# Optimization experiments

Measured on AMD Instinct MI355X. Metric: run time of the kernel, lower is better.

The kernel has to match this reference:

```python
import jax, jax.numpy as jnp
import numpy as np

B, T, E, H = 8, 2048, 1024, 64  # batch, seq_len(=block_size), embedding_size, head_size


def setup_inputs() -> dict:
    key = jax.random.key(0)
    k1, k2, k3, k4, k5 = jax.random.split(key, 5)
    x = jax.random.normal(k1, (B, T, E), dtype=jnp.float32)
    Wk = jax.random.normal(k2, (H, E), dtype=jnp.float32) * 0.02
    Wq = jax.random.normal(k3, (H, E), dtype=jnp.float32) * 0.02
    Wv = jax.random.normal(k4, (H, E), dtype=jnp.float32) * 0.02
    attention_mask = jax.random.randint(k5, (B, T), 0, 2).astype(jnp.int32)
    return {"x": x, "Wk": Wk, "Wq": Wq, "Wv": Wv, "attention_mask": attention_mask}


def reference(x, Wk, Wq, Wv, attention_mask):
    # Linear projections (nn.Linear with no bias: y = x @ W.T)
    k = jnp.einsum('bte,he->bth', x, Wk)
    q = jnp.einsum('bte,he->bth', x, Wq)
    v = jnp.einsum('bte,he->bth', x, Wv)
    scale = v.shape[2] ** -0.5  # head_size^-0.5, faithful to v.shape[2]**(-0.5)
    wei = jnp.einsum('bqh,bkh->bqk', q, k) * scale  # [B,T,T]
    # Causal mask (tril buffer) AND padding outer-product mask; the double-precision
    # outer product in the original just tests nonzero-ness, so a boolean AND is exact.
    causal = jnp.tril(jnp.ones((T, T), dtype=bool))  # [T,T]
    pad = (attention_mask[:, :, None] * attention_mask[:, None, :]) != 0  # [B,T,T]
    wei = jnp.where(causal[None, :, :] & pad, wei, -jnp.inf)
    wei = jax.nn.softmax(wei, axis=-1)
    wei = jnp.nan_to_num(wei)  # fully-masked rows -> 0 (matches torch.nan_to_num)
    # dropout in eval mode -> identity
    out = jnp.einsum('bqk,bkh->bqh', wei, v)
    return out
```

## Files before the change

kernel.cpp:

```cpp
#include <hip/hip_runtime.h>
#include <hip/hip_bf16.h>

typedef __bf16 bf16x8 __attribute__((ext_vector_type(8)));
typedef __bf16 bf16x4 __attribute__((ext_vector_type(4)));
typedef float  f32x4  __attribute__((ext_vector_type(4)));

#define LDP  72
#define KLDP 72
#define VLDP 72
#define PLDP 72

#define BAR() { asm volatile("s_waitcnt lgkmcnt(0)" ::: "memory"); __builtin_amdgcn_s_barrier(); }

__global__ __launch_bounds__(256) void wconv_kernel(
    const float* __restrict__ Wk, const float* __restrict__ Wq,
    const float* __restrict__ Wv, const int* __restrict__ mask,
    __bf16* __restrict__ wbf, unsigned* __restrict__ maskw)
{
    if (blockIdx.x == 192) {
        for (int wdx = threadIdx.x; wdx < 512; wdx += 256) {
            unsigned wv = 0;
            #pragma unroll
            for (int bit = 0; bit < 32; bit++)
                wv |= (mask[wdx * 32 + bit] != 0 ? 1u : 0u) << bit;
            maskw[wdx] = wv;
        }
        return;
    }
    int idx = blockIdx.x * 256 + threadIdx.x;
    int row = idx >> 8;
    int c4  = idx & 255;
    const float* wp = (row < 64) ? Wk + (size_t)row * 1024
                    : (row < 128) ? Wq + (size_t)(row - 64) * 1024
                                  : Wv + (size_t)(row - 128) * 1024;
    float4 f = *reinterpret_cast<const float4*>(wp + c4 * 4);
    bf16x4 v; v[0] = (__bf16)f.x; v[1] = (__bf16)f.y; v[2] = (__bf16)f.z; v[3] = (__bf16)f.w;
    *reinterpret_cast<bf16x4*>(&wbf[(size_t)row * 1024 + c4 * 4]) = v;
}

__global__ __launch_bounds__(1024) void proj_kernel(
    const float* __restrict__ x, const __bf16* __restrict__ wbf,
    __bf16* __restrict__ kbuf, __bf16* __restrict__ qbuf, __bf16* __restrict__ vtbuf)
{
    __shared__ __align__(16) __bf16 Slds[2][256 * LDP];
    __shared__ __align__(16) __bf16 Vtl[64 * LDP];

    const int tid  = threadIdx.x;
    const int lane = tid & 63;
    const int wid  = tid >> 6;
    const int wm   = wid >> 2;
    const int wn   = wid & 3;
    const int mbase = blockIdx.x * 64;

    const int cl = lane & 15;
    const int e0 = (lane >> 4) * 8;
    const int r0 = (lane >> 4) * 4;

    const int arow = tid >> 4, acg = tid & 15;
    const float* aptr = x + (size_t)(mbase + arow) * 1024 + acg * 4;

    float4 a0, a1;
    bf16x4 w0[3], w1[3];

#define ISSUE(aset, wset, kb) { \
    aset = *reinterpret_cast<const float4*>(aptr + (kb)); \
    _Pragma("unroll") \
    for (int i_ = 0; i_ < 3; i_++) { \
        int c_ = i_ * 1024 + tid; \
        wset[i_] = *reinterpret_cast<const bf16x4*>(&wbf[(size_t)(c_ >> 4) * 1024 + (kb) + (c_ & 15) * 4]); \
    } }

#define COMMIT(aset, wset, bufi) { \
    bf16x4 av_; \
    av_[0] = (__bf16)aset.x; av_[1] = (__bf16)aset.y; av_[2] = (__bf16)aset.z; av_[3] = (__bf16)aset.w; \
    *reinterpret_cast<bf16x4*>(&Slds[bufi][arow * LDP + acg * 4]) = av_; \
    _Pragma("unroll") \
    for (int i_ = 0; i_ < 3; i_++) { \
        int c_ = i_ * 1024 + tid; \
        *reinterpret_cast<bf16x4*>(&Slds[bufi][(64 + (c_ >> 4)) * LDP + (c_ & 15) * 4]) = wset[i_]; \
    } }

    f32x4 acc[3];
    #pragma unroll
    for (int n = 0; n < 3; n++) acc[n] = (f32x4){0.f, 0.f, 0.f, 0.f};

    ISSUE(a0, w0, 0);
    COMMIT(a0, w0, 0);
    ISSUE(a1, w1, 64);
    BAR();

    #pragma unroll 2
    for (int j = 0; j < 16; j++) {
        if (j < 14) {
            if (j & 1) { ISSUE(a1, w1, (j + 2) * 64); }
            else       { ISSUE(a0, w0, (j + 2) * 64); }
        }
        const __bf16* buf = Slds[j & 1];
        #pragma unroll
        for (int kk = 0; kk < 2; kk++) {
            bf16x8 a = *reinterpret_cast<const bf16x8*>(&buf[(wm * 16 + cl) * LDP + kk * 32 + e0]);
            #pragma unroll
            for (int nf = 0; nf < 3; nf++) {
                bf16x8 b = *reinterpret_cast<const bf16x8*>(&buf[(64 + wn * 48 + nf * 16 + cl) * LDP + kk * 32 + e0]);
                acc[nf] = __builtin_amdgcn_mfma_f32_16x16x32_bf16(a, b, acc[nf], 0, 0, 0);
            }
        }
        if (j < 15) {
            if (j & 1) { COMMIT(a0, w0, 0); }
            else       { COMMIT(a1, w1, 1); }
            BAR();
        }
    }
#undef ISSUE
#undef COMMIT

    #pragma unroll
    for (int nf = 0; nf < 3; nf++) {
        int c = wn * 48 + nf * 16 + cl;
        #pragma unroll
        for (int r = 0; r < 4; r++) {
            int mrel = wm * 16 + r0 + r;
            float v = acc[nf][r];
            if (c < 64)        kbuf[(size_t)(mbase + mrel) * 64 + c]         = (__bf16)v;
            else if (c < 128)  qbuf[(size_t)(mbase + mrel) * 64 + (c - 64)]  = (__bf16)v;
            else               Vtl[(c - 128) * LDP + mrel]                   = (__bf16)v;
        }
    }
    __syncthreads();
    {
        int b   = mbase >> 11;
        int tof = mbase & 2047;
        int h   = tid >> 4;
        int seg = tid & 15;
        bf16x4 v4 = *reinterpret_cast<const bf16x4*>(&Vtl[h * LDP + seg * 4]);
        *reinterpret_cast<bf16x4*>(&vtbuf[(size_t)b * 64 * 2048 + (size_t)h * 2048 + tof + seg * 4]) = v4;
    }
}

__global__ __launch_bounds__(128) void attn_kernel(
    const __bf16* __restrict__ qbuf, const __bf16* __restrict__ kbuf,
    const __bf16* __restrict__ vtbuf, const unsigned* __restrict__ maskw,
    float* __restrict__ out, float* __restrict__ accpart, float* __restrict__ mlpart,
    int nsplit, int tps)
{
    __shared__ __align__(16) __bf16 Klds[64 * KLDP];
    __shared__ __align__(16) __bf16 Vlds[64 * VLDP];
    __shared__ __align__(16) __bf16 Plds[2][2][16 * PLDP];

    const int tid  = threadIdx.x;
    const int lane = tid & 63;
    const int w    = tid >> 6;
    const int wg   = blockIdx.x;
    const int b    = wg & 7;
    const int rr_  = wg >> 3;
    const int qt   = rr_ & 31;
    const int sp   = rr_ >> 5;

    const int jbeg = sp * tps;
    const int jend = min((sp + 1) * tps, qt + 1);

    if (nsplit > 1 && jbeg >= jend) {
        for (int i = tid; i < 64; i += 128) {
            size_t mo = ((size_t)(b * nsplit + sp) * 2048 + qt * 64 + i) * 2;
            mlpart[mo] = -INFINITY; mlpart[mo + 1] = 0.f;
        }
        return;
    }

    const int cl = lane & 15;
    const int e0 = (lane >> 4) * 8;
    const int r0 = (lane >> 4) * 4;
    const int qs0 = qt * 64 + w * 16 + cl;
    const int qs1 = qs0 + 32;

    bf16x8 aq0[2], aq1[2];
    #pragma unroll
    for (int kk = 0; kk < 2; kk++) {
        aq0[kk] = *reinterpret_cast<const bf16x8*>(&qbuf[((size_t)b * 2048 + qs0) * 64 + kk * 32 + e0]);
        aq1[kk] = *reinterpret_cast<const bf16x8*>(&qbuf[((size_t)b * 2048 + qs1) * 64 + kk * 32 + e0]);
    }

    float m0 = -INFINITY, l0 = 0.f, m1 = -INFINITY, l1 = 0.f;
    f32x4 acc0[4], acc1[4];
    #pragma unroll
    for (int hf = 0; hf < 4; hf++) { acc0[hf] = (f32x4){0.f,0.f,0.f,0.f}; acc1[hf] = (f32x4){0.f,0.f,0.f,0.f}; }

    const __bf16* kb  = kbuf  + (size_t)b * 2048 * 64;
    const __bf16* vtb = vtbuf + (size_t)b * 64 * 2048;

    const int srow = tid >> 1;
    const int sc   = (tid & 1) * 32;
    bf16x8 stk[4], stv[4];

#define KV_ISSUE(jj) { _Pragma("unroll") for (int i_ = 0; i_ < 4; i_++) { \
    stk[i_] = *reinterpret_cast<const bf16x8*>(&kb[(size_t)((jj) * 64 + srow) * 64 + sc + i_ * 8]); \
    stv[i_] = *reinterpret_cast<const bf16x8*>(&vtb[(size_t)srow * 2048 + (jj) * 64 + sc + i_ * 8]); } }

#define KV_COMMIT() { _Pragma("unroll") for (int i_ = 0; i_ < 4; i_++) { \
    *reinterpret_cast<bf16x8*>(&Klds[srow * KLDP + sc + i_ * 8]) = stk[i_]; \
    *reinterpret_cast<bf16x8*>(&Vlds[srow * VLDP + sc + i_ * 8]) = stv[i_]; } }

#define SOFTMAX(S, mS, lS, accS, qsS, su) { \
    float tmax = -INFINITY; \
    _Pragma("unroll") for (int jf = 0; jf < 4; jf++) { \
        unsigned mw = (jf < 2) ? mw0 : mw1; \
        _Pragma("unroll") for (int r = 0; r < 4; r++) { \
            int kvl = jf * 16 + r0 + r; \
            bool ok = ((mw >> (kvl & 31)) & 1u) && (j * 64 + kvl <= qsS); \
            float sv = S[jf][r] * 0.125f; \
            sv = ok ? sv : -INFINITY; \
            S[jf][r] = sv; tmax = fmaxf(tmax, sv); } } \
    tmax = fmaxf(tmax, __shfl_xor(tmax, 16)); \
    tmax = fmaxf(tmax, __shfl_xor(tmax, 32)); \
    float mn = fmaxf(mS, tmax); \
    float alpha = (mn == -INFINITY) ? 1.0f : __expf(mS - mn); \
    float rs = 0.f; \
    _Pragma("unroll") for (int jf = 0; jf < 4; jf++) \
        _Pragma("unroll") for (int r = 0; r < 4; r++) { \
            float p = (mn == -INFINITY) ? 0.f : __expf(S[jf][r] - mn); \
            S[jf][r] = p; rs += p; } \
    rs += __shfl_xor(rs, 16); \
    rs += __shfl_xor(rs, 32); \
    lS = lS * alpha + rs; mS = mn; \
    _Pragma("unroll") for (int hf = 0; hf < 4; hf++) \
        _Pragma("unroll") for (int r = 0; r < 4; r++) accS[hf][r] *= alpha; \
    _Pragma("unroll") for (int jf = 0; jf < 4; jf++) { \
        bf16x4 p4; \
        _Pragma("unroll") for (int r = 0; r < 4; r++) p4[r] = (__bf16)S[jf][r]; \
        *reinterpret_cast<bf16x4*>(&Plds[w][su][cl * PLDP + jf * 16 + r0]) = p4; } }

    const int nt = jend - jbeg;
    KV_ISSUE(jbeg);
    KV_COMMIT();
    if (nt > 1) KV_ISSUE(jbeg + 1);
    BAR();

    for (int t = 0; t < nt; t++) {
        const int j = jbeg + t;

        f32x4 s0[4], s1[4];
        #pragma unroll
        for (int jf = 0; jf < 4; jf++) {
            f32x4 t0 = (f32x4){0.f,0.f,0.f,0.f}, t1 = (f32x4){0.f,0.f,0.f,0.f};
            #pragma unroll
            for (int kk = 0; kk < 2; kk++) {
                bf16x8 bk = *reinterpret_cast<const bf16x8*>(&Klds[(jf * 16 + cl) * KLDP + kk * 32 + e0]);
                t0 = __builtin_amdgcn_mfma_f32_16x16x32_bf16(bk, aq0[kk], t0, 0, 0, 0);
                t1 = __builtin_amdgcn_mfma_f32_16x16x32_bf16(bk, aq1[kk], t1, 0, 0, 0);
            }
            s0[jf] = t0; s1[jf] = t1;
        }

        const unsigned mw0 = maskw[b * 64 + j * 2];
        const unsigned mw1 = maskw[b * 64 + j * 2 + 1];
        SOFTMAX(s0, m0, l0, acc0, qs0, 0);
        SOFTMAX(s1, m1, l1, acc1, qs1, 1);

        #pragma unroll
        for (int kk = 0; kk < 2; kk++) {
            bf16x8 p0 = *reinterpret_cast<const bf16x8*>(&Plds[w][0][cl * PLDP + kk * 32 + e0]);
            bf16x8 p1 = *reinterpret_cast<const bf16x8*>(&Plds[w][1][cl * PLDP + kk * 32 + e0]);
            #pragma unroll
            for (int hf = 0; hf < 4; hf++) {
                bf16x8 av = *reinterpret_cast<const bf16x8*>(&Vlds[(hf * 16 + cl) * VLDP + kk * 32 + e0]);
                acc0[hf] = __builtin_amdgcn_mfma_f32_16x16x32_bf16(av, p0, acc0[hf], 0, 0, 0);
                acc1[hf] = __builtin_amdgcn_mfma_f32_16x16x32_bf16(av, p1, acc1[hf], 0, 0, 0);
            }
        }

        BAR();
        if (t + 1 < nt) {
            KV_COMMIT();
            if (t + 2 < nt) KV_ISSUE(j + 2);
            BAR();
        }
    }
#undef KV_ISSUE
#undef KV_COMMIT
#undef SOFTMAX

    const bool mq0 = (maskw[b * 64 + (qs0 >> 5)] >> (qs0 & 31)) & 1u;
    const bool mq1 = (maskw[b * 64 + (qs1 >> 5)] >> (qs1 & 31)) & 1u;
    if (nsplit == 1) {
        #pragma unroll
        for (int hf = 0; hf < 4; hf++)
            #pragma unroll
            for (int r = 0; r < 4; r++) {
                float v0 = (l0 > 0.f && mq0) ? acc0[hf][r] / l0 : 0.f;
                float v1 = (l1 > 0.f && mq1) ? acc1[hf][r] / l1 : 0.f;
                out[((size_t)b * 2048 + qs0) * 64 + hf * 16 + r0 + r] = v0;
                out[((size_t)b * 2048 + qs1) * 64 + hf * 16 + r0 + r] = v1;
            }
    } else {
        #pragma unroll
        for (int hf = 0; hf < 4; hf++)
            #pragma unroll
            for (int r = 0; r < 4; r++) {
                accpart[((size_t)(b * nsplit + sp) * 2048 + qs0) * 64 + hf * 16 + r0 + r] = acc0[hf][r];
                accpart[((size_t)(b * nsplit + sp) * 2048 + qs1) * 64 + hf * 16 + r0 + r] = acc1[hf][r];
            }
        if (lane < 16) {
            size_t mo0 = ((size_t)(b * nsplit + sp) * 2048 + qs0) * 2;
            size_t mo1 = ((size_t)(b * nsplit + sp) * 2048 + qs1) * 2;
            mlpart[mo0] = m0; mlpart[mo0 + 1] = l0;
            mlpart[mo1] = m1; mlpart[mo1 + 1] = l1;
        }
    }
}

template<int NS>
__global__ __launch_bounds__(256) void combine_kernel(
    const float* __restrict__ accpart, const float* __restrict__ mlpart,
    const unsigned* __restrict__ maskw, float* __restrict__ out)
{
    int idx = blockIdx.x * 256 + threadIdx.x;
    int qglob = idx >> 6;
    int h = idx & 63;
    int b = qglob >> 11;
    int qrow = qglob & 2047;

    if (!((maskw[b * 64 + (qrow >> 5)] >> (qrow & 31)) & 1u)) { out[idx] = 0.f; return; }

    float m_s[NS], l_s[NS];
    float M = -INFINITY;
    #pragma unroll
    for (int s = 0; s < NS; s++) {
        size_t mo = ((size_t)(b * NS + s) * 2048 + qrow) * 2;
        m_s[s] = mlpart[mo];
        l_s[s] = mlpart[mo + 1];
        M = fmaxf(M, m_s[s]);
    }
    if (M == -INFINITY) { out[idx] = 0.f; return; }

    float L = 0.f, O = 0.f;
    #pragma unroll
    for (int s = 0; s < NS; s++) {
        float wgt = (m_s[s] == -INFINITY) ? 0.f : __expf(m_s[s] - M);
        L += l_s[s] * wgt;
        O += wgt * accpart[((size_t)(b * NS + s) * 2048 + qrow) * 64 + h];
    }
    out[idx] = (L > 0.f) ? O / L : 0.f;
}

extern "C" void kernel_launch(void* const* d_in, const int* in_sizes, int n_in,
                              void* d_out, int out_size, void* d_ws, size_t ws_size,
                              hipStream_t stream) {
    const float* x  = (const float*)d_in[0];
    const float* Wk = (const float*)d_in[1];
    const float* Wq = (const float*)d_in[2];
    const float* Wv = (const float*)d_in[3];
    const int* mask = (const int*)d_in[4];
    float* out = (float*)d_out;

    const size_t NTOK = 8 * 2048;
    __bf16* kbuf  = (__bf16*)d_ws;
    __bf16* qbuf  = kbuf + NTOK * 64;
    __bf16* vtbuf = qbuf + NTOK * 64;
    __bf16* wbf   = vtbuf + (size_t)8 * 64 * 2048;
    unsigned* maskw = (unsigned*)(wbf + (size_t)192 * 1024);
    const size_t base_bytes = NTOK * 64 * 2 * 2 + (size_t)8 * 64 * 2048 * 2
                            + (size_t)192 * 1024 * 2 + 512 * 4;

    const size_t acc_per_split = NTOK * 64 * 4;
    const size_t ml_per_split  = NTOK * 2 * 4;
    int nsplit = 1;
    if (ws_size >= base_bytes + 4 * (acc_per_split + ml_per_split))      nsplit = 4;
    else if (ws_size >= base_bytes + 2 * (acc_per_split + ml_per_split)) nsplit = 2;

    float* accpart = (float*)((char*)d_ws + base_bytes);
    float* mlpart  = accpart + NTOK * 64 * nsplit;

    wconv_kernel<<<193, 256, 0, stream>>>(Wk, Wq, Wv, mask, wbf, maskw);
    proj_kernel<<<256, 1024, 0, stream>>>(x, wbf, kbuf, qbuf, vtbuf);
    attn_kernel<<<8 * 32 * nsplit, 128, 0, stream>>>(
        qbuf, kbuf, vtbuf, maskw, out, accpart, mlpart, nsplit, 32 / nsplit);
    if (nsplit == 4)
        combine_kernel<4><<<(16384 * 64) / 256, 256, 0, stream>>>(accpart, mlpart, maskw, out);
    else if (nsplit == 2)
        combine_kernel<2><<<(16384 * 64) / 256, 256, 0, stream>>>(accpart, mlpart, maskw, out);
}
```

Baseline: 58.21 us.

## Add lazy softmax rescale, MFMA priority hints, and skip masked-row partial writes

The online softmax now rescales the running max, sum and accumulators only when some lane's new tile max exceeds the stored max by more than a threshold of 8 (FA4-style lazy rescaling). This removes the per-tile exp and accumulator multiplies in the common case. s_setprio raises wave priority around the MFMA blocks. In the split path, accpart/mlpart stores are skipped for padded query rows, and combine skips loads for empty splits. The lazy threshold lets unnormalized exponentials grow up to e^8, which is safe in fp32 but adds bf16 rounding risk on P.

```diff
diff --git a/kernel.cpp b/kernel.cpp
--- a/kernel.cpp
+++ b/kernel.cpp
@@ -161,8 +161,11 @@
 
     if (nsplit > 1 && jbeg >= jend) {
         for (int i = tid; i < 64; i += 128) {
-            size_t mo = ((size_t)(b * nsplit + sp) * 2048 + qt * 64 + i) * 2;
-            mlpart[mo] = -INFINITY; mlpart[mo + 1] = 0.f;
+            int qrow = qt * 64 + i;
+            if ((maskw[b * 64 + (qrow >> 5)] >> (qrow & 31)) & 1u) {
+                size_t mo = ((size_t)(b * nsplit + sp) * 2048 + qrow) * 2;
+                mlpart[mo] = -INFINITY; mlpart[mo + 1] = 0.f;
+            }
         }
         return;
     }
@@ -212,18 +215,21 @@
             S[jf][r] = sv; tmax = fmaxf(tmax, sv); } } \
     tmax = fmaxf(tmax, __shfl_xor(tmax, 16)); \
     tmax = fmaxf(tmax, __shfl_xor(tmax, 32)); \
-    float mn = fmaxf(mS, tmax); \
-    float alpha = (mn == -INFINITY) ? 1.0f : __expf(mS - mn); \
+    if (!__all(tmax <= mS + 8.f)) { \
+        float mn = fmaxf(mS, tmax);             \
+        float alpha = __expf(mS - mn);          \
+        lS *= alpha; mS = mn; \
+        _Pragma("unroll") for (int hf = 0; hf < 4; hf++) \
+            _Pragma("unroll") for (int r = 0; r < 4; r++) accS[hf][r] *= alpha; \
+    } \
     float rs = 0.f; \
     _Pragma("unroll") for (int jf = 0; jf < 4; jf++) \
         _Pragma("unroll") for (int r = 0; r < 4; r++) { \
-            float p = (mn == -INFINITY) ? 0.f : __expf(S[jf][r] - mn); \
+            float p = (mS == -INFINITY) ? 0.f : __expf(S[jf][r] - mS); \
             S[jf][r] = p; rs += p; } \
     rs += __shfl_xor(rs, 16); \
     rs += __shfl_xor(rs, 32); \
-    lS = lS * alpha + rs; mS = mn; \
-    _Pragma("unroll") for (int hf = 0; hf < 4; hf++) \
-        _Pragma("unroll") for (int r = 0; r < 4; r++) accS[hf][r] *= alpha; \
+    lS += rs; \
     _Pragma("unroll") for (int jf = 0; jf < 4; jf++) { \
         bf16x4 p4; \
         _Pragma("unroll") for (int r = 0; r < 4; r++) p4[r] = (__bf16)S[jf][r]; \
@@ -239,6 +245,7 @@
         const int j = jbeg + t;
 
         f32x4 s0[4], s1[4];
+        __builtin_amdgcn_s_setprio(1);
         #pragma unroll
         for (int jf = 0; jf < 4; jf++) {
             f32x4 t0 = (f32x4){0.f,0.f,0.f,0.f}, t1 = (f32x4){0.f,0.f,0.f,0.f};
@@ -250,12 +257,14 @@
             }
             s0[jf] = t0; s1[jf] = t1;
         }
+        __builtin_amdgcn_s_setprio(0);
 
         const unsigned mw0 = maskw[b * 64 + j * 2];
         const unsigned mw1 = maskw[b * 64 + j * 2 + 1];
         SOFTMAX(s0, m0, l0, acc0, qs0, 0);
         SOFTMAX(s1, m1, l1, acc1, qs1, 1);
 
+        __builtin_amdgcn_s_setprio(1);
         #pragma unroll
         for (int kk = 0; kk < 2; kk++) {
             bf16x8 p0 = *reinterpret_cast<const bf16x8*>(&Plds[w][0][cl * PLDP + kk * 32 + e0]);
@@ -267,6 +276,7 @@
                 acc1[hf] = __builtin_amdgcn_mfma_f32_16x16x32_bf16(av, p1, acc1[hf], 0, 0, 0);
             }
         }
+        __builtin_amdgcn_s_setprio(0);
 
         BAR();
         if (t + 1 < nt) {
@@ -292,18 +302,29 @@
                 out[((size_t)b * 2048 + qs1) * 64 + hf * 16 + r0 + r] = v1;
             }
     } else {
-        #pragma unroll
-        for (int hf = 0; hf < 4; hf++)
-            #pragma unroll
-            for (int r = 0; r < 4; r++) {
-                accpart[((size_t)(b * nsplit + sp) * 2048 + qs0) * 64 + hf * 16 + r0 + r] = acc0[hf][r];
-                accpart[((size_t)(b * nsplit + sp) * 2048 + qs1) * 64 + hf * 16 + r0 + r] = acc1[hf][r];
-            }
+        if (mq0) {
+            #pragma unroll
+            for (int hf = 0; hf < 4; hf++)
+                #pragma unroll
+                for (int r = 0; r < 4; r++)
+                    accpart[((size_t)(b * nsplit + sp) * 2048 + qs0) * 64 + hf * 16 + r0 + r] = acc0[hf][r];
+        }
+        if (mq1) {
+            #pragma unroll
+            for (int hf = 0; hf < 4; hf++)
+                #pragma unroll
+                for (int r = 0; r < 4; r++)
+                    accpart[((size_t)(b * nsplit + sp) * 2048 + qs1) * 64 + hf * 16 + r0 + r] = acc1[hf][r];
+        }
         if (lane < 16) {
-            size_t mo0 = ((size_t)(b * nsplit + sp) * 2048 + qs0) * 2;
-            size_t mo1 = ((size_t)(b * nsplit + sp) * 2048 + qs1) * 2;
-            mlpart[mo0] = m0; mlpart[mo0 + 1] = l0;
-            mlpart[mo1] = m1; mlpart[mo1 + 1] = l1;
+            if (mq0) {
+                size_t mo0 = ((size_t)(b * nsplit + sp) * 2048 + qs0) * 2;
+                mlpart[mo0] = m0; mlpart[mo0 + 1] = l0;
+            }
+            if (mq1) {
+                size_t mo1 = ((size_t)(b * nsplit + sp) * 2048 + qs1) * 2;
+                mlpart[mo1] = m1; mlpart[mo1 + 1] = l1;
+            }
         }
     }
 }
@@ -335,9 +356,11 @@
     float L = 0.f, O = 0.f;
     #pragma unroll
     for (int s = 0; s < NS; s++) {
-        float wgt = (m_s[s] == -INFINITY) ? 0.f : __expf(m_s[s] - M);
-        L += l_s[s] * wgt;
-        O += wgt * accpart[((size_t)(b * NS + s) * 2048 + qrow) * 64 + h];
+        if (m_s[s] > -INFINITY) {
+            float wgt = __expf(m_s[s] - M);
+            L += l_s[s] * wgt;
+            O += wgt * accpart[((size_t)(b * NS + s) * 2048 + qrow) * 64 + h];
+        }
     }
     out[idx] = (L > 0.f) ? O / L : 0.f;
 }
```

Measured after the change: 58.03 us. Within noise of the previous version (-0.3%).
